# Performance work log

Hardware: AMD Instinct MI355X
Metric: run time of the kernel (lower is better)

## Reference

```python
import jax, jax.numpy as jnp
import numpy as np

B, S, DIM, HD = 4, 1024, 2048, 128
H = DIM // HD  # 16 heads
GN_EPS = 1e-3  # Keras GroupNormalization default epsilon


def setup_inputs() -> dict:
    key = jax.random.key(0)
    ks = jax.random.split(key, 8)
    x = jax.random.normal(ks[0], (B, S, DIM), dtype=jnp.float32)
    k = jax.random.normal(ks[1], (B, S, DIM), dtype=jnp.float32)
    v = jax.random.normal(ks[2], (B, S, DIM), dtype=jnp.float32)
    # One shared QKV projection weight per head (dict.fromkeys bug in source
    # makes Q, K, V use the SAME Dense layer). Keras Dense: y = x @ W, W:(in,out)
    Wh = jax.random.normal(ks[3], (H, HD, HD), dtype=jnp.float32) / np.sqrt(HD)
    wg_w = jax.random.normal(ks[4], (DIM, DIM), dtype=jnp.float32) / np.sqrt(DIM)
    wo_w = jax.random.normal(ks[5], (DIM, DIM), dtype=jnp.float32) / np.sqrt(DIM)
    gn_gamma = jnp.ones((DIM,), dtype=jnp.float32)
    gn_beta = jnp.zeros((DIM,), dtype=jnp.float32)
    return {"x": x, "k": k, "v": v, "Wh": Wh, "wg_w": wg_w, "wo_w": wo_w,
            "gn_gamma": gn_gamma, "gn_beta": gn_beta}


def _decay_masks(n_heads, seq_len):
    # Source: band_part(gamma**(i-j), 0, -1) then transpose ->
    # D[h, i, j] = gamma_h ** (j - i) for j <= i, else 0.
    gam = 1.0 - 2.0 ** (-5.0 - jnp.arange(n_heads, dtype=jnp.float32))  # (H,)
    idx = jnp.arange(seq_len, dtype=jnp.float32)
    expo = idx[None, :] - idx[:, None]               # (S,S): j - i
    D = jnp.where(expo[None, :, :] <= 0,
                  gam[:, None, None] ** expo[None, :, :], 0.0)  # (H,S,S)
    # TF: D /= reduce_sum(D, 1)**0.5 broadcasts row-sums along the COLUMN axis
    return D / jnp.sqrt(D.sum(axis=-1))[:, None, :]


def reference(x, k, v, Wh, wg_w, wo_w, gn_gamma, gn_beta):
    b, s, dim = x.shape
    h, hd, _ = Wh.shape
    # split last axis into contiguous per-head chunks
    xh = x.reshape(b, s, h, hd)
    kh = k.reshape(b, s, h, hd)
    vh = v.reshape(b, s, h, hd)
    # Q, K, V share the same per-head weight (faithful to dict.fromkeys)
    Q = jnp.einsum('bshd,hde->bshe', xh, Wh)
    K = jnp.einsum('bshd,hde->bshe', kh, Wh)
    V = jnp.einsum('bshd,hde->bshe', vh, Wh)
    scores = jnp.einsum('bshe,bthe->bhst', Q, K) / jnp.sqrt(jnp.float32(hd))
    Dn = _decay_masks(h, s)                          # (H,S,S)
    masked = scores * Dn[None, :, :, :]              # (B,H,S,S)
    # source reduces over axis 0 == BATCH, then abs, then clamp at 1
    A = jnp.maximum(jnp.abs(masked.sum(axis=0)), 1.0)  # (H,S,S)
    O = jnp.einsum('hst,bthe->bshe', A, V).reshape(b, s, dim)
    # GroupNormalization(groups=1): per-token layernorm over channels
    mu = O.mean(axis=-1, keepdims=True)
    var = O.var(axis=-1, keepdims=True)
    Y = (O - mu) / jnp.sqrt(var + GN_EPS) * gn_gamma + gn_beta
    W = jax.nn.relu(x @ wg_w)                        # gated branch
    return (W * Y) @ wo_w
```

## Files before the change

### kernel.cpp

```cpp
#include <hip/hip_runtime.h>
#include <math.h>

constexpr int Bc = 4, Sc = 1024, Dc = 2048, HDc = 128, Hc = 16;
constexpr int BSc = Bc * Sc;
constexpr int KQKc = Bc * HDc;
#define GN_EPS 1e-3f

typedef __bf16 bf16x8 __attribute__((ext_vector_type(8)));
typedef __bf16 bf16x4 __attribute__((ext_vector_type(4)));
typedef float f32x4 __attribute__((ext_vector_type(4)));

constexpr size_t OFF_Q   = 0;
constexpr size_t OFF_K   = OFF_Q + (size_t)Hc * Sc * KQKc / 2;
constexpr size_t OFF_VB  = OFF_K + (size_t)Hc * Sc * KQKc / 2;
constexpr size_t OFF_VT  = OFF_VB + (size_t)BSc * Dc / 2;
constexpr size_t OFF_A   = OFF_VT + (size_t)BSc * Dc / 2;
constexpr size_t OFF_O   = OFF_A + (size_t)Hc * Sc * Sc / 2;
constexpr size_t OFF_CT  = OFF_O + (size_t)BSc * Dc;
constexpr size_t OFF_PN  = OFF_CT + (size_t)Hc * Sc;
constexpr size_t OFF_XB  = OFF_PN + (size_t)Hc * Sc;
constexpr size_t OFF_WGT = OFF_XB + (size_t)BSc * Dc / 2;
constexpr size_t OFF_WOT = OFF_WGT + (size_t)Dc * Dc / 2;
constexpr size_t OFF_SUF = OFF_WOT + (size_t)Dc * Dc / 2;
constexpr size_t OFF_T   = OFF_SUF + (size_t)64 * 9 * HDc;
constexpr size_t OFF_WHT = OFF_T + (size_t)64 * 8 * HDc;
constexpr size_t OFF_STAT= OFF_WHT + (size_t)Hc * HDc * HDc / 2;

#define GLOAD_LDS16(gp, lp)                                               \
  __builtin_amdgcn_global_load_lds(                                       \
      (const __attribute__((address_space(1))) void*)(gp),                \
      (__attribute__((address_space(3))) void*)(lp), 16, 0, 0)


constexpr int ABUFE = 128 * 64;
constexpr int BBUFE = 128 * 64;
constexpr int MG_LDS = (3 * ABUFE + 2 * BBUFE) * 2;
constexpr int PJ_LDS = 4 * 8192 * 2;

template <int ASTR, int BSTR, int NF = 4, int MF = 4>
__device__ __forceinline__ void mfma_loop128(const __bf16* __restrict__ Abase,
                                             const __bf16* __restrict__ Bbase,
                                             const int ntk,
                                             __bf16* As, __bf16* Bs,
                                             const int wave, const int lane,
                                             f32x4 acc[MF][NF]) {
  constexpr int NH = NF / 2;
  constexpr int MH = MF / 2;
  constexpr int ABE = MF * 2048;
  const int wr = wave >> 1, wc = wave & 1;
  const int lr = lane >> 2;
  const int lkx = ((lane & 3) ^ ((lane >> 3) & 3)) * 8;
  const int rl = lane & 15, kq = lane >> 4;
  const int swo = rl * 32 + ((kq ^ ((rl >> 1) & 3)) * 8);

#define VMW_MF()                                                            \
  do {                                                                      \
    if constexpr (MF == 4)                                                  \
      asm volatile("s_waitcnt vmcnt(4)" ::: "memory");                      \
    else                                                                    \
      asm volatile("s_waitcnt vmcnt(2)" ::: "memory");                      \
  } while (0)

#define SA_(i, kt, bsel) do {                                               \
    const int ci_ = (i) * 4 + wave;                                         \
    GLOAD_LDS16(Abase + (size_t)((ci_ >> 1) * 16 + lr) * ASTR               \
                    + (kt) * 64 + (ci_ & 1) * 32 + lkx,                     \
                As + (bsel) * ABE + ci_ * 512);                             \
  } while (0)
#define SB_(j, kt, bsel) do {                                               \
    const int ci_ = (j) * 4 + wave;                                         \
    GLOAD_LDS16(Bbase + (size_t)((ci_ >> 1) * 16 + lr) * BSTR               \
                    + (kt) * 64 + (ci_ & 1) * 32 + lkx,                     \
                Bs + (bsel) * BBUFE + ci_ * 512);                           \
  } while (0)

  #pragma unroll
  for (int i = 0; i < MF; ++i) SA_(i, 0, 0);
  #pragma unroll
  for (int j = 0; j < NF; ++j) SB_(j, 0, 0);
  #pragma unroll
  for (int i = 0; i < MF; ++i) SA_(i, 1, 1);
  __builtin_amdgcn_sched_barrier(0);
  VMW_MF();
  __builtin_amdgcn_sched_barrier(0);
  __builtin_amdgcn_s_barrier();

  int cbA = 0;
  for (int t = 0; t < ntk; ++t) {
    const int sbA = (cbA + 2 >= 3) ? cbA - 1 : cbA + 2;
    const __bf16* Ac = As + cbA * ABE;
    const __bf16* Bc = Bs + (t & 1) * BBUFE;
    bf16x8 a[MF][2], b[NF][2];
    #pragma unroll
    for (int m = 0; m < MH; ++m)
      #pragma unroll
      for (int kc = 0; kc < 2; ++kc)
        a[m][kc] = *(const bf16x8*)&Ac[((wr * MF + m) * 2 + kc) * 512 + swo];
    #pragma unroll
    for (int n = 0; n < NH; ++n)
      #pragma unroll
      for (int kc = 0; kc < 2; ++kc)
        b[n][kc] = *(const bf16x8*)&Bc[((wc * NF + n) * 2 + kc) * 512 + swo];
    #pragma unroll
    for (int m = MH; m < MF; ++m)
      #pragma unroll
      for (int kc = 0; kc < 2; ++kc)
        a[m][kc] = *(const bf16x8*)&Ac[((wr * MF + m) * 2 + kc) * 512 + swo];
    #pragma unroll
    for (int n = NH; n < NF; ++n)
      #pragma unroll
      for (int kc = 0; kc < 2; ++kc)
        b[n][kc] = *(const bf16x8*)&Bc[((wc * NF + n) * 2 + kc) * 512 + swo];
    if (t + 1 < ntk) {
      #pragma unroll
      for (int j = 0; j < NF; ++j) SB_(j, t + 1, (t + 1) & 1);
    }
    if (t + 2 < ntk) {
      #pragma unroll
      for (int i = 0; i < MF; ++i) SA_(i, t + 2, sbA);
    }
    __builtin_amdgcn_sched_barrier(0);
    __builtin_amdgcn_s_setprio(1);
    #pragma unroll
    for (int kc = 0; kc < 2; ++kc)
      #pragma unroll
      for (int m = 0; m < MH; ++m)
        #pragma unroll
        for (int n = 0; n < NH; ++n)
          acc[m][n] = __builtin_amdgcn_mfma_f32_16x16x32_bf16(
              a[m][kc], b[n][kc], acc[m][n], 0, 0, 0);
    __builtin_amdgcn_s_setprio(0);
    __builtin_amdgcn_sched_barrier(0);
    __builtin_amdgcn_s_setprio(1);
    #pragma unroll
    for (int kc = 0; kc < 2; ++kc)
      #pragma unroll
      for (int m = MH; m < MF; ++m)
        #pragma unroll
        for (int n = 0; n < NH; ++n)
          acc[m][n] = __builtin_amdgcn_mfma_f32_16x16x32_bf16(
              a[m][kc], b[n][kc], acc[m][n], 0, 0, 0);
    __builtin_amdgcn_s_setprio(0);
    __builtin_amdgcn_sched_barrier(0);
    __builtin_amdgcn_s_setprio(1);
    #pragma unroll
    for (int kc = 0; kc < 2; ++kc)
      #pragma unroll
      for (int m = 0; m < MH; ++m)
        #pragma unroll
        for (int n = NH; n < NF; ++n)
          acc[m][n] = __builtin_amdgcn_mfma_f32_16x16x32_bf16(
              a[m][kc], b[n][kc], acc[m][n], 0, 0, 0);
    __builtin_amdgcn_s_setprio(0);
    __builtin_amdgcn_sched_barrier(0);
    __builtin_amdgcn_s_setprio(1);
    #pragma unroll
    for (int kc = 0; kc < 2; ++kc)
      #pragma unroll
      for (int m = MH; m < MF; ++m)
        #pragma unroll
        for (int n = NH; n < NF; ++n)
          acc[m][n] = __builtin_amdgcn_mfma_f32_16x16x32_bf16(
              a[m][kc], b[n][kc], acc[m][n], 0, 0, 0);
    __builtin_amdgcn_s_setprio(0);
    __builtin_amdgcn_sched_barrier(0);
    asm volatile("s_waitcnt lgkmcnt(0)" ::: "memory");
    __builtin_amdgcn_sched_barrier(0);
    if (t + 2 < ntk) {
      VMW_MF();
    } else if (t + 1 < ntk) {
      asm volatile("s_waitcnt vmcnt(0)" ::: "memory");
    }
    __builtin_amdgcn_sched_barrier(0);
    __builtin_amdgcn_s_barrier();
    cbA = (cbA + 1 >= 3) ? 0 : cbA + 1;
  }
#undef SA_
#undef SB_
#undef VMW_MF
}

__global__ __launch_bounds__(256) void k_tables(float* __restrict__ ct,
                                                float* __restrict__ pn,
                                                float* __restrict__ TP,
                                                float* __restrict__ STAT) {
  int idx = blockIdx.x * 256 + threadIdx.x;
  int h = idx >> 10, t = idx & 1023;
  double gamma = 1.0 - exp2(-(double)(5 + h));
  double l2g = log2(gamma);
  double r = 1.0 / gamma;
  double rowsum = (exp2(-(double)(t + 1) * l2g) - 1.0) / (r - 1.0);
  ct[idx] = (float)(exp2((double)t * l2g) / sqrt(rowsum));
  pn[idx] = (float)exp2(-(double)t * l2g);
  float4 z4 = {0.f, 0.f, 0.f, 0.f};
  *(float4*)(TP + (size_t)idx * 4) = z4;
  if (idx < BSc * 2) STAT[idx] = 0.f;
}

__global__ __launch_bounds__(256) void k_cast8(const float* __restrict__ src,
                                               __bf16* __restrict__ dst) {
  size_t i = ((size_t)blockIdx.x * 256 + threadIdx.x) * 8;
  float4 a = *(const float4*)(src + i);
  float4 b = *(const float4*)(src + i + 4);
  bf16x8 o;
  o[0] = (__bf16)a.x; o[1] = (__bf16)a.y; o[2] = (__bf16)a.z; o[3] = (__bf16)a.w;
  o[4] = (__bf16)b.x; o[5] = (__bf16)b.y; o[6] = (__bf16)b.z; o[7] = (__bf16)b.w;
  *(bf16x8*)(dst + i) = o;
}

__global__ __launch_bounds__(256) void k_castT2(const float* __restrict__ s0,
                                                const float* __restrict__ s1,
                                                __bf16* __restrict__ d0,
                                                __bf16* __restrict__ d1) {
  __shared__ float t[32][33];
  const int bx = blockIdx.x, by = blockIdx.y;
  const float* src = blockIdx.z ? s1 : s0;
  __bf16* dst = blockIdx.z ? d1 : d0;
  const int tid = threadIdx.x;
  const int lx = tid & 31, ly = tid >> 5;
  #pragma unroll
  for (int r = 0; r < 32; r += 8)
    t[ly + r][lx] = src[(size_t)(by * 32 + ly + r) * Dc + bx * 32 + lx];
  __syncthreads();
  #pragma unroll
  for (int r = 0; r < 32; r += 8)
    dst[(size_t)(bx * 32 + ly + r) * Dc + by * 32 + lx] = (__bf16)t[lx][ly + r];
}

__global__ __launch_bounds__(256) void k_whT(const float* __restrict__ Wh,
                                             __bf16* __restrict__ WhT) {
  __shared__ float t[32][33];
  const int h = blockIdx.z;
  const int d0 = blockIdx.x * 32, e0 = blockIdx.y * 32;
  const int tid = threadIdx.x;
  const int lx = tid & 31, ly = tid >> 5;
  #pragma unroll
  for (int r = 0; r < 32; r += 8)
    t[ly + r][lx] = Wh[(size_t)h * HDc * HDc + (d0 + ly + r) * HDc + e0 + lx];
  __syncthreads();
  #pragma unroll
  for (int r = 0; r < 32; r += 8)
    WhT[(size_t)h * HDc * HDc + (e0 + ly + r) * HDc + d0 + lx] =
        (__bf16)t[lx][ly + r];
}

__global__ __launch_bounds__(256, 2) void k_projm(const __bf16* __restrict__ Xb,
                                                  const float* __restrict__ kf,
                                                  const float* __restrict__ vf,
                                                  const __bf16* __restrict__ WhT,
                                                  __bf16* __restrict__ Qo,
                                                  __bf16* __restrict__ Ko,
                                                  __bf16* __restrict__ Vt,
                                                  float* __restrict__ TP) {
  extern __shared__ __bf16 lds[];
  __bf16* Xs = lds;
  __bf16* Ws = lds + 2 * 8192;
  const int r0 = blockIdx.x * 128;
  const int h = blockIdx.y;
  const int z = blockIdx.z;
  const __bf16* wsrc = WhT + (size_t)h * HDc * HDc;
  const int tid = threadIdx.x;
  const int wave = tid >> 6, lane = tid & 63;
  const int wr = wave >> 1, wc = wave & 1;
  const int lr = lane >> 2;
  const int lkx = ((lane & 3) ^ ((lane >> 3) & 3)) * 8;
  const int rl = lane & 15, kq = lane >> 4;
  const int swo = rl * 32 + ((kq ^ ((rl >> 1) & 3)) * 8);
  #pragma unroll
  for (int kt = 0; kt < 2; ++kt) {
    #pragma unroll
    for (int i = 0; i < 4; ++i) {
      const int ci = i * 4 + wave;
      const int row = (ci >> 1) * 16 + lr;
      const int ko = kt * 64 + (ci & 1) * 32 + lkx;
      GLOAD_LDS16(wsrc + (size_t)row * HDc + ko, Ws + kt * 8192 + ci * 512);
    }
  }
  if (z == 0) {
    #pragma unroll
    for (int kt = 0; kt < 2; ++kt) {
      #pragma unroll
      for (int i = 0; i < 4; ++i) {
        const int ci = i * 4 + wave;
        const int row = (ci >> 1) * 16 + lr;
        const int ko = kt * 64 + (ci & 1) * 32 + lkx;
        GLOAD_LDS16(Xb + (size_t)(r0 + row) * Dc + h * HDc + ko,
                    Xs + kt * 8192 + ci * 512);
      }
    }
  } else {
    const float* fsrc = (z == 1) ? kf : vf;
    #pragma unroll
    for (int kt = 0; kt < 2; ++kt) {
      #pragma unroll
      for (int i = 0; i < 4; ++i) {
        const int ci = i * 4 + wave;
        const int row = (ci >> 1) * 16 + lr;
        const int ko = kt * 64 + (ci & 1) * 32 + lkx;
        const float* gp = fsrc + (size_t)(r0 + row) * Dc + h * HDc + ko;
        f32x4 f0 = *(const f32x4*)gp;
        f32x4 f1 = *(const f32x4*)(gp + 4);
        bf16x8 o;
        o[0] = (__bf16)f0[0]; o[1] = (__bf16)f0[1];
        o[2] = (__bf16)f0[2]; o[3] = (__bf16)f0[3];
        o[4] = (__bf16)f1[0]; o[5] = (__bf16)f1[1];
        o[6] = (__bf16)f1[2]; o[7] = (__bf16)f1[3];
        *(bf16x8*)&Xs[kt * 8192 + ci * 512 + lane * 8] = o;
      }
    }
  }
  __builtin_amdgcn_sched_barrier(0);
  asm volatile("s_waitcnt vmcnt(0) lgkmcnt(0)" ::: "memory");
  __builtin_amdgcn_sched_barrier(0);
  __builtin_amdgcn_s_barrier();
  f32x4 acc[4][4] = {{}};
  #pragma unroll
  for (int kt = 0; kt < 2; ++kt) {
    bf16x8 a[4][2], b[4][2];
    #pragma unroll
    for (int m = 0; m < 4; ++m)
      #pragma unroll
      for (int kc = 0; kc < 2; ++kc)
        a[m][kc] =
            *(const bf16x8*)&Xs[kt * 8192 + ((wr * 4 + m) * 2 + kc) * 512 + swo];
    #pragma unroll
    for (int n = 0; n < 4; ++n)
      #pragma unroll
      for (int kc = 0; kc < 2; ++kc)
        b[n][kc] =
            *(const bf16x8*)&Ws[kt * 8192 + ((wc * 4 + n) * 2 + kc) * 512 + swo];
    #pragma unroll
    for (int kc = 0; kc < 2; ++kc)
      #pragma unroll
      for (int m = 0; m < 4; ++m)
        #pragma unroll
        for (int n = 0; n < 4; ++n)
          acc[m][n] = __builtin_amdgcn_mfma_f32_16x16x32_bf16(
              a[m][kc], b[n][kc], acc[m][n], 0, 0, 0);
  }
  if (z == 2) {
    __bf16* tl = lds;
    __syncthreads();
    #pragma unroll
    for (int mi = 0; mi < 4; ++mi) {
      #pragma unroll
      for (int nj = 0; nj < 4; ++nj) {
        const int col = wc * 64 + nj * 16 + rl;
        const int rrb = wr * 64 + mi * 16 + kq * 4;
        bf16x4 v4;
        v4[0] = (__bf16)acc[mi][nj][0];
        v4[1] = (__bf16)acc[mi][nj][1];
        v4[2] = (__bf16)acc[mi][nj][2];
        v4[3] = (__bf16)acc[mi][nj][3];
        *(bf16x4*)&tl[col * 132 + rrb] = v4;
      }
    }
    __syncthreads();
    const int e = tid >> 1, rh = (tid & 1) * 64;
    const int bh2 = (r0 >> 10) * 16 + h;
    const int jj = (r0 & 1023) >> 7;
    const int sb = r0 & 1023;
    float colsum = 0.f;
    #pragma unroll
    for (int j = 0; j < 8; ++j) {
      bf16x8 v = *(const bf16x8*)&tl[e * 132 + rh + j * 8];
      #pragma unroll
      for (int q = 0; q < 8; ++q) colsum += (float)v[q];
      *(bf16x8*)&Vt[((size_t)bh2 * HDc + e) * Sc + sb + rh + j * 8] = v;
    }
    atomicAdd(&TP[((size_t)bh2 * 8 + jj) * HDc + e], colsum);
  } else {
    __bf16* dst = (z == 0) ? Qo : Ko;
    #pragma unroll
    for (int mi = 0; mi < 4; ++mi) {
      #pragma unroll
      for (int nj = 0; nj < 4; ++nj) {
        const int col = wc * 64 + nj * 16 + rl;
        #pragma unroll
        for (int r = 0; r < 4; ++r) {
          const int row = r0 + wr * 64 + mi * 16 + kq * 4 + r;
          const int s = row & 1023, bb = row >> 10;
          dst[((size_t)(h * Sc + s) * Bc + bb) * HDc + col] =
              (__bf16)acc[mi][nj][r];
        }
      }
    }
  }
}

__global__ __launch_bounds__(128) void k_vscan(const float* __restrict__ T,
                                               float* __restrict__ SufV) {
  const int bh = blockIdx.x;
  const int e = threadIdx.x;
  float acc = 0.f;
  SufV[((size_t)bh * 9 + 8) * HDc + e] = 0.f;
  for (int jj = 7; jj >= 1; --jj) {
    acc += T[((size_t)bh * 8 + jj) * HDc + e];
    SufV[((size_t)bh * 9 + jj) * HDc + e] = acc;
  }
}

__global__ __launch_bounds__(256, 2) void k_ssm(const __bf16* __restrict__ Q,
                                                const __bf16* __restrict__ Kb,
                                                const float* __restrict__ ct,
                                                const float* __restrict__ pn,
                                                __bf16* __restrict__ A) {
  const int bx = blockIdx.x, by = blockIdx.y;
  int r, c, half;
  if (by == 8)       { r = bx; c = bx; half = 1; }
  else if (bx > by)  { r = bx; c = by; half = 1; }
  else               { r = by; c = bx; half = 0; }
  extern __shared__ __bf16 lds[];
  __bf16* As = lds;
  __bf16* Bs = lds + 3 * ABUFE;
  const int h = blockIdx.z;
  const int s0 = r * 128;
  const int t0 = c * 128 + half * 64;
  const int tid = threadIdx.x;
  __bf16* Ah = A + (size_t)h * Sc * Sc;
  const int wave = tid >> 6, lane = tid & 63;
  f32x4 acc[4][2] = {{}};
  mfma_loop128<KQKc, KQKc, 2>(Q + (size_t)(h * Sc + s0) * KQKc,
                              Kb + (size_t)(h * Sc + t0) * KQKc, KQKc / 64,
                              As, Bs, wave, lane, acc);
  const int wr = wave >> 1, wc = wave & 1;
  const int rl = lane & 15, kq = lane >> 4;
  const float rs = 0.088388347648318447f;
  #pragma unroll
  for (int mi = 0; mi < 4; ++mi) {
    #pragma unroll
    for (int nj = 0; nj < 2; ++nj) {
      const int t = t0 + wc * 32 + nj * 16 + rl;
      const float ctv = ct[h * Sc + t] * rs;
      #pragma unroll
      for (int rr = 0; rr < 4; ++rr) {
        const int s = s0 + wr * 64 + mi * 16 + kq * 4 + rr;
        float v = 1.0f;
        if (t <= s) v = fmaxf(fabsf(ctv * pn[h * Sc + s] * acc[mi][nj][rr]), 1.0f);
        Ah[(size_t)s * Sc + t] = (__bf16)v;
      }
    }
  }
}

__global__ __launch_bounds__(256, 2) void k_avm(const __bf16* __restrict__ A,
                                                const __bf16* __restrict__ Vt,
                                                const float* __restrict__ SufV,
                                                float* __restrict__ O,
                                                float* __restrict__ STAT) {
  extern __shared__ __bf16 lds[];
  __bf16* As = lds;
  __bf16* Bs = lds + 3 * ABUFE;
  const int lid = (int)blockIdx.z * 8 + (int)blockIdx.x;
  const int slot = lid & 255;
  const int bh = slot >> 2;
  const int itile = (lid < 256) ? (slot & 3) : 7 - (slot & 3);
  const int bb = bh >> 4, h = bh & 15;
  const int s0 = itile * 128;
  const int tid = threadIdx.x;
  const int wave = tid >> 6, lane = tid & 63;
  const int wr = wave >> 1, wc = wave & 1;
  const int rl = lane & 15, kq = lane >> 4;
  f32x4 acc[4][4] = {{}};
  mfma_loop128<Sc, Sc>(A + (size_t)(h * Sc + s0) * Sc,
                       Vt + (size_t)bh * HDc * Sc, (itile + 1) * 2, As, Bs,
                       wave, lane, acc);
  const float* sufr = SufV + ((size_t)bh * 9 + (itile + 1)) * HDc;
  #pragma unroll
  for (int mi = 0; mi < 4; ++mi) {
    #pragma unroll
    for (int r = 0; r < 4; ++r) {
      const int s = s0 + wr * 64 + mi * 16 + kq * 4 + r;
      const size_t orow = (size_t)(bb * Sc + s);
      float vs = 0.f, vq = 0.f;
      #pragma unroll
      for (int nj = 0; nj < 4; ++nj) {
        const int e = wc * 64 + nj * 16 + rl;
        const float v = acc[mi][nj][r] + sufr[e];
        O[orow * Dc + h * HDc + e] = v;
        vs += v;
        vq += v * v;
      }
      #pragma unroll
      for (int m = 1; m < 16; m <<= 1) {
        vs += __shfl_xor(vs, m);
        vq += __shfl_xor(vq, m);
      }
      if (rl == 0) {
        atomicAdd(&STAT[orow * 2], vs);
        atomicAdd(&STAT[orow * 2 + 1], vq);
      }
    }
  }
}

__global__ __launch_bounds__(256, 2) void k_mgemm(const __bf16* __restrict__ Ab,
                                                  const __bf16* __restrict__ Bt,
                                                  const float* __restrict__ Y,
                                                  const float* __restrict__ gw,
                                                  const float* __restrict__ bw,
                                                  const float* __restrict__ STAT,
                                                  __bf16* __restrict__ Gout,
                                                  float* __restrict__ Fout,
                                                  int mode) {
  extern __shared__ __bf16 lds[];
  __bf16* As = lds;
  __bf16* Bs = lds + 3 * ABUFE;
  int wid = blockIdx.y * gridDim.x + blockIdx.x;
  wid = (wid & 7) * 64 + (wid >> 3);
  const int r0 = (wid >> 4) * 128;
  const int c0 = (wid & 15) * 128;
  const int tid = threadIdx.x;
  const int wave = tid >> 6, lane = tid & 63;
  f32x4 acc[4][4] = {{}};
  mfma_loop128<Dc, Dc>(Ab + (size_t)r0 * Dc, Bt + (size_t)c0 * Dc, Dc / 64,
                       As, Bs, wave, lane, acc);
  const int wr = wave >> 1, wc = wave & 1;
  const int rl = lane & 15, kq = lane >> 4;
  if (mode == 0) {
    #pragma unroll
    for (int mi = 0; mi < 4; ++mi) {
      #pragma unroll
      for (int r = 0; r < 4; ++r) {
        const int row = r0 + wr * 64 + mi * 16 + kq * 4 + r;
        const float mu = STAT[(size_t)row * 2] * (1.0f / Dc);
        const float va = STAT[(size_t)row * 2 + 1] * (1.0f / Dc) - mu * mu;
        const float inv = rsqrtf(va + GN_EPS);
        #pragma unroll
        for (int nj = 0; nj < 4; ++nj) {
          const int col = c0 + wc * 64 + nj * 16 + rl;
          const size_t idx = (size_t)row * Dc + col;
          const float yv = (Y[idx] - mu) * inv * gw[col] + bw[col];
          Gout[idx] = (__bf16)(fmaxf(acc[mi][nj][r], 0.f) * yv);
        }
      }
    }
  } else {
    #pragma unroll
    for (int mi = 0; mi < 4; ++mi) {
      #pragma unroll
      for (int nj = 0; nj < 4; ++nj) {
        const int col = c0 + wc * 64 + nj * 16 + rl;
        #pragma unroll
        for (int r = 0; r < 4; ++r) {
          const int row = r0 + wr * 64 + mi * 16 + kq * 4 + r;
          Fout[(size_t)row * Dc + col] = acc[mi][nj][r];
        }
      }
    }
  }
}

extern "C" void kernel_launch(void* const* d_in, const int* in_sizes, int n_in,
                              void* d_out, int out_size, void* d_ws, size_t ws_size,
                              hipStream_t stream) {
  const float* x  = (const float*)d_in[0];
  const float* k  = (const float*)d_in[1];
  const float* v  = (const float*)d_in[2];
  const float* Wh = (const float*)d_in[3];
  const float* wg = (const float*)d_in[4];
  const float* wo = (const float*)d_in[5];
  const float* gg = (const float*)d_in[6];
  const float* gb = (const float*)d_in[7];
  float* ws = (float*)d_ws;
  __bf16* Q   = (__bf16*)(ws + OFF_Q);
  __bf16* Kp  = (__bf16*)(ws + OFF_K);
  __bf16* Vt  = (__bf16*)(ws + OFF_VT);
  __bf16* A   = (__bf16*)(ws + OFF_A);
  float*  O   = ws + OFF_O;
  float*  CT  = ws + OFF_CT;
  float*  PN  = ws + OFF_PN;
  __bf16* XB  = (__bf16*)(ws + OFF_XB);
  __bf16* WGT = (__bf16*)(ws + OFF_WGT);
  __bf16* WOT = (__bf16*)(ws + OFF_WOT);
  float*  SUF = ws + OFF_SUF;
  float*  TP  = ws + OFF_T;
  __bf16* WHT = (__bf16*)(ws + OFF_WHT);
  float*  STAT= ws + OFF_STAT;
  __bf16* G   = (__bf16*)(ws + OFF_Q);

  static bool attr_done = false;
  if (!attr_done) {
    (void)hipFuncSetAttribute((const void*)k_mgemm,
                              hipFuncAttributeMaxDynamicSharedMemorySize,
                              MG_LDS);
    (void)hipFuncSetAttribute((const void*)k_projm,
                              hipFuncAttributeMaxDynamicSharedMemorySize,
                              PJ_LDS);
    (void)hipFuncSetAttribute((const void*)k_ssm,
                              hipFuncAttributeMaxDynamicSharedMemorySize,
                              MG_LDS);
    (void)hipFuncSetAttribute((const void*)k_avm,
                              hipFuncAttributeMaxDynamicSharedMemorySize,
                              MG_LDS);
    attr_done = true;
  }

  k_tables<<<Hc * Sc / 256, 256, 0, stream>>>(CT, PN, TP, STAT);
  k_cast8<<<(BSc * Dc) / (256 * 8), 256, 0, stream>>>(x, XB);
  k_castT2<<<dim3(Dc / 32, Dc / 32, 2), 256, 0, stream>>>(wg, wo, WGT, WOT);
  k_whT<<<dim3(4, 4, Hc), 256, 0, stream>>>(Wh, WHT);
  k_projm<<<dim3(BSc / 128, Hc, 3), 256, PJ_LDS, stream>>>(XB, k, v, WHT,
                                                           Q, Kp, Vt, TP);
  k_vscan<<<Bc * Hc, 128, 0, stream>>>(TP, SUF);
  k_ssm<<<dim3(8, 9, Hc), 256, MG_LDS, stream>>>(Q, Kp, CT, PN, A);
  k_avm<<<dim3(8, 1, Bc * Hc), 256, MG_LDS, stream>>>(A, Vt, SUF, O, STAT);
  k_mgemm<<<dim3(16, 32), 256, MG_LDS, stream>>>(XB, WGT, O, gg, gb, STAT, G,
                                                 nullptr, 0);
  k_mgemm<<<dim3(16, 32), 256, MG_LDS, stream>>>(G, WOT, nullptr, nullptr,
                                                 nullptr, nullptr, nullptr,
                                                 (float*)d_out, 1);
}
```

Measured before the change: 342.7 us.

## Fuse table setup into cast, inline suffix scan into AV, store O as bf16

```diff
diff --git a/kernel.cpp b/kernel.cpp
--- a/kernel.cpp
+++ b/kernel.cpp
@@ -180,25 +180,12 @@
 #undef VMW_MF
 }
 
-__global__ __launch_bounds__(256) void k_tables(float* __restrict__ ct,
+__global__ __launch_bounds__(256) void k_cast8t(const float* __restrict__ src,
+                                                __bf16* __restrict__ dst,
+                                                float* __restrict__ ct,
                                                 float* __restrict__ pn,
                                                 float* __restrict__ TP,
                                                 float* __restrict__ STAT) {
-  int idx = blockIdx.x * 256 + threadIdx.x;
-  int h = idx >> 10, t = idx & 1023;
-  double gamma = 1.0 - exp2(-(double)(5 + h));
-  double l2g = log2(gamma);
-  double r = 1.0 / gamma;
-  double rowsum = (exp2(-(double)(t + 1) * l2g) - 1.0) / (r - 1.0);
-  ct[idx] = (float)(exp2((double)t * l2g) / sqrt(rowsum));
-  pn[idx] = (float)exp2(-(double)t * l2g);
-  float4 z4 = {0.f, 0.f, 0.f, 0.f};
-  *(float4*)(TP + (size_t)idx * 4) = z4;
-  if (idx < BSc * 2) STAT[idx] = 0.f;
-}
-
-__global__ __launch_bounds__(256) void k_cast8(const float* __restrict__ src,
-                                               __bf16* __restrict__ dst) {
   size_t i = ((size_t)blockIdx.x * 256 + threadIdx.x) * 8;
   float4 a = *(const float4*)(src + i);
   float4 b = *(const float4*)(src + i + 4);
@@ -206,6 +193,19 @@
   o[0] = (__bf16)a.x; o[1] = (__bf16)a.y; o[2] = (__bf16)a.z; o[3] = (__bf16)a.w;
   o[4] = (__bf16)b.x; o[5] = (__bf16)b.y; o[6] = (__bf16)b.z; o[7] = (__bf16)b.w;
   *(bf16x8*)(dst + i) = o;
+  if (blockIdx.x < 64) {
+    int idx = blockIdx.x * 256 + threadIdx.x;
+    int h = idx >> 10, t = idx & 1023;
+    double gamma = 1.0 - exp2(-(double)(5 + h));
+    double l2g = log2(gamma);
+    double r = 1.0 / gamma;
+    double rowsum = (exp2(-(double)(t + 1) * l2g) - 1.0) / (r - 1.0);
+    ct[idx] = (float)(exp2((double)t * l2g) / sqrt(rowsum));
+    pn[idx] = (float)exp2(-(double)t * l2g);
+    float4 z4 = {0.f, 0.f, 0.f, 0.f};
+    *(float4*)(TP + (size_t)idx * 4) = z4;
+    if (idx < BSc * 2) STAT[idx] = 0.f;
+  }
 }
 
 __global__ __launch_bounds__(256) void k_castT2(const float* __restrict__ s0,
@@ -385,18 +385,6 @@
         }
       }
     }
-  }
-}
-
-__global__ __launch_bounds__(128) void k_vscan(const float* __restrict__ T,
-                                               float* __restrict__ SufV) {
-  const int bh = blockIdx.x;
-  const int e = threadIdx.x;
-  float acc = 0.f;
-  SufV[((size_t)bh * 9 + 8) * HDc + e] = 0.f;
-  for (int jj = 7; jj >= 1; --jj) {
-    acc += T[((size_t)bh * 8 + jj) * HDc + e];
-    SufV[((size_t)bh * 9 + jj) * HDc + e] = acc;
   }
 }
 
@@ -445,8 +433,8 @@
 
 __global__ __launch_bounds__(256, 2) void k_avm(const __bf16* __restrict__ A,
                                                 const __bf16* __restrict__ Vt,
-                                                const float* __restrict__ SufV,
-                                                float* __restrict__ O,
+                                                const float* __restrict__ TP,
+                                                __bf16* __restrict__ O,
                                                 float* __restrict__ STAT) {
   extern __shared__ __bf16 lds[];
   __bf16* As = lds;
@@ -461,11 +449,19 @@
   const int wave = tid >> 6, lane = tid & 63;
   const int wr = wave >> 1, wc = wave & 1;
   const int rl = lane & 15, kq = lane >> 4;
+  float suf4[4];
+  #pragma unroll
+  for (int nj = 0; nj < 4; ++nj) {
+    const int e = wc * 64 + nj * 16 + rl;
+    float s = 0.f;
+    for (int jj = itile + 1; jj < 8; ++jj)
+      s += TP[((size_t)bh * 8 + jj) * HDc + e];
+    suf4[nj] = s;
+  }
   f32x4 acc[4][4] = {{}};
   mfma_loop128<Sc, Sc>(A + (size_t)(h * Sc + s0) * Sc,
                        Vt + (size_t)bh * HDc * Sc, (itile + 1) * 2, As, Bs,
                        wave, lane, acc);
-  const float* sufr = SufV + ((size_t)bh * 9 + (itile + 1)) * HDc;
   #pragma unroll
   for (int mi = 0; mi < 4; ++mi) {
     #pragma unroll
@@ -476,8 +472,8 @@
       #pragma unroll
       for (int nj = 0; nj < 4; ++nj) {
         const int e = wc * 64 + nj * 16 + rl;
-        const float v = acc[mi][nj][r] + sufr[e];
-        O[orow * Dc + h * HDc + e] = v;
+        const float v = acc[mi][nj][r] + suf4[nj];
+        O[orow * Dc + h * HDc + e] = (__bf16)v;
         vs += v;
         vq += v * v;
       }
@@ -496,7 +492,7 @@
 
 __global__ __launch_bounds__(256, 2) void k_mgemm(const __bf16* __restrict__ Ab,
                                                   const __bf16* __restrict__ Bt,
-                                                  const float* __restrict__ Y,
+                                                  const __bf16* __restrict__ Y,
                                                   const float* __restrict__ gw,
                                                   const float* __restrict__ bw,
                                                   const float* __restrict__ STAT,
@@ -530,7 +526,7 @@
         for (int nj = 0; nj < 4; ++nj) {
           const int col = c0 + wc * 64 + nj * 16 + rl;
           const size_t idx = (size_t)row * Dc + col;
-          const float yv = (Y[idx] - mu) * inv * gw[col] + bw[col];
+          const float yv = ((float)Y[idx] - mu) * inv * gw[col] + bw[col];
           Gout[idx] = (__bf16)(fmaxf(acc[mi][nj][r], 0.f) * yv);
         }
       }
@@ -567,13 +563,12 @@
   __bf16* Kp  = (__bf16*)(ws + OFF_K);
   __bf16* Vt  = (__bf16*)(ws + OFF_VT);
   __bf16* A   = (__bf16*)(ws + OFF_A);
-  float*  O   = ws + OFF_O;
+  __bf16* O   = (__bf16*)(ws + OFF_O);
   float*  CT  = ws + OFF_CT;
   float*  PN  = ws + OFF_PN;
   __bf16* XB  = (__bf16*)(ws + OFF_XB);
   __bf16* WGT = (__bf16*)(ws + OFF_WGT);
   __bf16* WOT = (__bf16*)(ws + OFF_WOT);
-  float*  SUF = ws + OFF_SUF;
   float*  TP  = ws + OFF_T;
   __bf16* WHT = (__bf16*)(ws + OFF_WHT);
   float*  STAT= ws + OFF_STAT;
@@ -596,15 +591,14 @@
     attr_done = true;
   }
 
-  k_tables<<<Hc * Sc / 256, 256, 0, stream>>>(CT, PN, TP, STAT);
-  k_cast8<<<(BSc * Dc) / (256 * 8), 256, 0, stream>>>(x, XB);
+  k_cast8t<<<(BSc * Dc) / (256 * 8), 256, 0, stream>>>(x, XB, CT, PN, TP,
+                                                       STAT);
   k_castT2<<<dim3(Dc / 32, Dc / 32, 2), 256, 0, stream>>>(wg, wo, WGT, WOT);
   k_whT<<<dim3(4, 4, Hc), 256, 0, stream>>>(Wh, WHT);
   k_projm<<<dim3(BSc / 128, Hc, 3), 256, PJ_LDS, stream>>>(XB, k, v, WHT,
                                                            Q, Kp, Vt, TP);
-  k_vscan<<<Bc * Hc, 128, 0, stream>>>(TP, SUF);
   k_ssm<<<dim3(8, 9, Hc), 256, MG_LDS, stream>>>(Q, Kp, CT, PN, A);
-  k_avm<<<dim3(8, 1, Bc * Hc), 256, MG_LDS, stream>>>(A, Vt, SUF, O, STAT);
+  k_avm<<<dim3(8, 1, Bc * Hc), 256, MG_LDS, stream>>>(A, Vt, TP, O, STAT);
   k_mgemm<<<dim3(16, 32), 256, MG_LDS, stream>>>(XB, WGT, O, gg, gb, STAT, G,
                                                  nullptr, 0);
   k_mgemm<<<dim3(16, 32), 256, MG_LDS, stream>>>(G, WOT, nullptr, nullptr,
```

Result: faster. 328.1 us (-4.3%).
